# Performance work log

Measured on AMD Instinct MI355X. Metric: run time of the kernel, lower is better.

Reference implementation:

```python
import jax, jax.numpy as jnp
import numpy as np

LAMBDA_COOR = 5.0
LAMBDA_NOOBJ = 0.5


def setup_inputs() -> dict:
    key = jax.random.key(0)
    k1, k2 = jax.random.split(key)
    B, W, H, C = 128, 256, 256, 5
    outputs = jax.random.normal(k1, (B, W, H, C), dtype=jnp.float32)
    targets = jax.random.normal(k2, (B, W, H, C), dtype=jnp.float32)
    return {"outputs": outputs, "targets": targets}


def reference(outputs, targets):
    # channel layout per cell: (conf, x, y, w, h)
    conf_pred = outputs[..., 0]
    conf_gt = targets[..., 0]
    obj_mask = conf_gt > 0
    # sum of squared coord errors (x, y, w, h) per cell: [B, W, H]
    coord_sq = jnp.sum((outputs[..., 1:] - targets[..., 1:]) ** 2, axis=-1)
    obj_loss = LAMBDA_COOR * coord_sq + (conf_pred - 1.0) ** 2
    noobj_loss = LAMBDA_NOOBJ * conf_pred ** 2
    loss = jnp.sum(jnp.where(obj_mask, obj_loss, noobj_loss))
    return loss / outputs.shape[0]
```

## Files before the change

kernel.cpp:

```cpp
#include <hip/hip_runtime.h>

#define LAMBDA_COOR 5.0f
#define LAMBDA_NOOBJ 0.5f

__global__ __launch_bounds__(256) void yolo_loss_kernel(
    const float* __restrict__ outp, const float* __restrict__ tgt,
    float* __restrict__ loss, int n_groups, float inv_b)
{
    int tid = blockIdx.x * blockDim.x + threadIdx.x;
    int stride = gridDim.x * blockDim.x;
    float acc = 0.0f;

    for (int g = tid; g < n_groups; g += stride) {
        const float4* o4 = (const float4*)(outp + (size_t)g * 20);
        const float4* t4 = (const float4*)(tgt + (size_t)g * 20);
        float o[20], t[20];
        #pragma unroll
        for (int i = 0; i < 5; ++i) {
            float4 a = o4[i];
            float4 b = t4[i];
            o[4*i+0] = a.x; o[4*i+1] = a.y; o[4*i+2] = a.z; o[4*i+3] = a.w;
            t[4*i+0] = b.x; t[4*i+1] = b.y; t[4*i+2] = b.z; t[4*i+3] = b.w;
        }
        #pragma unroll
        for (int c = 0; c < 4; ++c) {
            const float* oc = o + 5*c;
            const float* tc = t + 5*c;
            float conf_p = oc[0];
            float coord = 0.0f;
            #pragma unroll
            for (int k = 1; k < 5; ++k) {
                float d = oc[k] - tc[k];
                coord += d * d;
            }
            float obj   = LAMBDA_COOR * coord + (conf_p - 1.0f) * (conf_p - 1.0f);
            float noobj = LAMBDA_NOOBJ * conf_p * conf_p;
            acc += (tc[0] > 0.0f) ? obj : noobj;
        }
    }

    #pragma unroll
    for (int off = 32; off > 0; off >>= 1)
        acc += __shfl_down(acc, off, 64);

    __shared__ float wave_sums[4];
    int lane = threadIdx.x & 63;
    int wid  = threadIdx.x >> 6;
    if (lane == 0) wave_sums[wid] = acc;
    __syncthreads();

    if (threadIdx.x == 0) {
        float s = wave_sums[0] + wave_sums[1] + wave_sums[2] + wave_sums[3];
        atomicAdd(loss, s * inv_b);
    }
}

extern "C" void kernel_launch(void* const* d_in, const int* in_sizes, int n_in,
                              void* d_out, int out_size, void* d_ws, size_t ws_size,
                              hipStream_t stream) {
    const float* outputs = (const float*)d_in[0];
    const float* targets = (const float*)d_in[1];
    float* loss = (float*)d_out;

    const int n_elems  = in_sizes[0];
    const int n_groups = n_elems / 20;
    const float inv_b  = 1.0f / 128.0f;

    hipMemsetAsync(d_out, 0, sizeof(float), stream);

    const int threads = 256;
    const int blocks  = 2048;
    yolo_loss_kernel<<<blocks, threads, 0, stream>>>(
        outputs, targets, loss, n_groups, inv_b);
}
```

Measured before the change: 332.5 us.

## Read inputs as coalesced float4 stream with per-element cell-confidence lookup

Each thread now reads one contiguous float4 per step instead of five float4s spanning a 20-float group. Adjacent lanes therefore touch adjacent 16-byte chunks, which makes the global loads fully coalesced, and the loop is unrolled four-wide to keep more loads in flight. Each element works out its cell position by dividing by 5 and fetches the target confidence of its cell (or the next cell) with extra scalar loads. This adds integer division and redundant cached loads of the target in exchange for a better memory access pattern. Launch bounds also request higher occupancy.

```diff
diff --git a/kernel.cpp b/kernel.cpp
--- a/kernel.cpp
+++ b/kernel.cpp
@@ -3,39 +3,76 @@
 #define LAMBDA_COOR 5.0f
 #define LAMBDA_NOOBJ 0.5f
 
-__global__ __launch_bounds__(256) void yolo_loss_kernel(
+__global__ __launch_bounds__(256, 8) void yolo_loss_kernel(
     const float* __restrict__ outp, const float* __restrict__ tgt,
-    float* __restrict__ loss, int n_groups, float inv_b)
+    float* __restrict__ loss, int n4, int n_elems, float inv_b)
 {
-    int tid = blockIdx.x * blockDim.x + threadIdx.x;
-    int stride = gridDim.x * blockDim.x;
+    const int tid = blockIdx.x * blockDim.x + threadIdx.x;
+    const int nth = gridDim.x * blockDim.x;
+    const float4* __restrict__ o4 = (const float4*)outp;
+    const float4* __restrict__ t4 = (const float4*)tgt;
+
     float acc = 0.0f;
 
-    for (int g = tid; g < n_groups; g += stride) {
-        const float4* o4 = (const float4*)(outp + (size_t)g * 20);
-        const float4* t4 = (const float4*)(tgt + (size_t)g * 20);
-        float o[20], t[20];
+    int i = tid;
+    for (; i + 3 * nth < n4; i += 4 * nth) {
+        float4 o[4], t[4];
         #pragma unroll
-        for (int i = 0; i < 5; ++i) {
-            float4 a = o4[i];
-            float4 b = t4[i];
-            o[4*i+0] = a.x; o[4*i+1] = a.y; o[4*i+2] = a.z; o[4*i+3] = a.w;
-            t[4*i+0] = b.x; t[4*i+1] = b.y; t[4*i+2] = b.z; t[4*i+3] = b.w;
+        for (int u = 0; u < 4; ++u) {
+            o[u] = o4[i + u * nth];
+            t[u] = t4[i + u * nth];
         }
+
+        float cg0[4], cg1[4];
+        int rem0[4];
         #pragma unroll
-        for (int c = 0; c < 4; ++c) {
-            const float* oc = o + 5*c;
-            const float* tc = t + 5*c;
-            float conf_p = oc[0];
-            float coord = 0.0f;
+        for (int u = 0; u < 4; ++u) {
+            int j0  = (i + u * nth) * 4;
+            int ci0 = (int)((unsigned)j0 / 5u) * 5;
+            rem0[u] = j0 - ci0;
+            cg0[u]  = tgt[ci0];
+            int ci1 = ci0 + 5;
+            cg1[u]  = (ci1 < n_elems) ? tgt[ci1] : 0.0f;
+        }
+
+        #pragma unroll
+        for (int u = 0; u < 4; ++u) {
+            float oe[4] = {o[u].x, o[u].y, o[u].z, o[u].w};
+            float te[4] = {t[u].x, t[u].y, t[u].z, t[u].w};
             #pragma unroll
-            for (int k = 1; k < 5; ++k) {
-                float d = oc[k] - tc[k];
-                coord += d * d;
+            for (int e = 0; e < 4; ++e) {
+                int   r      = rem0[u] + e;
+                float cg     = (r >= 5) ? cg1[u] : cg0[u];
+                bool  isconf = (r == 0) | (r == 5);
+                float d      = oe[e] - te[e];
+                float dm1    = oe[e] - 1.0f;
+                float obj    = isconf ? dm1 * dm1 : LAMBDA_COOR * d * d;
+                float nob    = isconf ? LAMBDA_NOOBJ * oe[e] * oe[e] : 0.0f;
+                acc += (cg > 0.0f) ? obj : nob;
             }
-            float obj   = LAMBDA_COOR * coord + (conf_p - 1.0f) * (conf_p - 1.0f);
-            float noobj = LAMBDA_NOOBJ * conf_p * conf_p;
-            acc += (tc[0] > 0.0f) ? obj : noobj;
+        }
+    }
+
+    for (; i < n4; i += nth) {
+        float4 o = o4[i], t = t4[i];
+        int j0  = i * 4;
+        int ci0 = (int)((unsigned)j0 / 5u) * 5;
+        int rem = j0 - ci0;
+        float cg0 = tgt[ci0];
+        int ci1 = ci0 + 5;
+        float cg1 = (ci1 < n_elems) ? tgt[ci1] : 0.0f;
+        float oe[4] = {o.x, o.y, o.z, o.w};
+        float te[4] = {t.x, t.y, t.z, t.w};
+        #pragma unroll
+        for (int e = 0; e < 4; ++e) {
+            int   r      = rem + e;
+            float cg     = (r >= 5) ? cg1 : cg0;
+            bool  isconf = (r == 0) | (r == 5);
+            float d      = oe[e] - te[e];
+            float dm1    = oe[e] - 1.0f;
+            float obj    = isconf ? dm1 * dm1 : LAMBDA_COOR * d * d;
+            float nob    = isconf ? LAMBDA_NOOBJ * oe[e] * oe[e] : 0.0f;
+            acc += (cg > 0.0f) ? obj : nob;
         }
     }
 
@@ -62,14 +99,14 @@
     const float* targets = (const float*)d_in[1];
     float* loss = (float*)d_out;
 
-    const int n_elems  = in_sizes[0];
-    const int n_groups = n_elems / 20;
-    const float inv_b  = 1.0f / 128.0f;
+    const int n_elems = in_sizes[0];
+    const int n4      = n_elems / 4;
+    const float inv_b = 1.0f / 128.0f;
 
     hipMemsetAsync(d_out, 0, sizeof(float), stream);
 
     const int threads = 256;
     const int blocks  = 2048;
     yolo_loss_kernel<<<blocks, threads, 0, stream>>>(
-        outputs, targets, loss, n_groups, inv_b);
+        outputs, targets, loss, n4, n_elems, inv_b);
 }
```

Measured after the change: 337.0 us. About the same (+1.3%).
